# Performance work log

Hardware: AMD Instinct MI355X
Metric: run time of the kernel (lower is better)

The kernel has to match this reference:

```python
import jax, jax.numpy as jnp
import numpy as np

B, S, D_MODEL, N_HEADS = 2, 2048, 1024, 16
HEAD_DIM = D_MODEL // N_HEADS  # 64
SCALE = HEAD_DIM ** -0.5
MASK_FILL = -1e9


def setup_inputs() -> dict:
    key = jax.random.key(0)
    k1, k2, k3 = jax.random.split(key, 3)
    x = jax.random.normal(k1, (B, S, D_MODEL), dtype=jnp.float32)
    # nn.Linear weight [3*d_att, d_model], trunc_normal std=0.02 style init
    W_qkv = jax.random.normal(k2, (3 * D_MODEL, D_MODEL), dtype=jnp.float32) * 0.02
    # boolean attention mask over the full [b, s_q, h, t_k] score tensor (True = keep)
    mask = jax.random.bernoulli(k3, p=0.9, shape=(B, S, N_HEADS, S))
    return {"x": x, "W_qkv": W_qkv, "mask": mask}


def reference(x, W_qkv, mask):
    b, s, dm = x.shape
    h, d = N_HEADS, HEAD_DIM
    # fused QKV projection (no bias): [b,s,3*dm] -> [b,s,3,h,d]
    qkv = jnp.einsum('bsm,nm->bsn', x, W_qkv).reshape(b, s, 3, h, d)
    q, k, v = qkv[:, :, 0], qkv[:, :, 1], qkv[:, :, 2]
    # scores: [b, s_q, h, t_k]
    attn = jnp.einsum('bshd,bthd->bsht', q, k) * SCALE
    attn = jnp.where(mask, attn, MASK_FILL)
    attn = jax.nn.softmax(attn, axis=-1)
    # out[b,t,h,d] = sum_s attn[b,t,h,s] * v[b,s,h,d]  (original einsum 'b s h d, b t h s -> b t h d')
    out = jnp.einsum('bshd,bths->bthd', v, attn)
    return out.reshape(b, s, h * d)  # proj is Identity (d_out=None)
```

## Files before the change

kernel.cpp:

```cpp
#include <hip/hip_runtime.h>

#define S_   2048
#define DM_  1024
#define NH_  16
#define HD_  64
#define NQ_  3072
#define KDIM 1024

typedef __attribute__((ext_vector_type(8))) short  shortx8;
typedef __attribute__((ext_vector_type(4))) float  floatx4;

#define AS1 __attribute__((address_space(1)))
#define AS3 __attribute__((address_space(3)))

__device__ __forceinline__ unsigned short f2bf(float f) {
  unsigned u = __float_as_uint(f);
  u += 0x7FFFu + ((u >> 16) & 1u);
  return (unsigned short)(u >> 16);
}

__device__ __forceinline__ void gld_lds16(const void* g, unsigned short* l) {
  __builtin_amdgcn_global_load_lds((const AS1 void*)g, (AS3 void*)l, 16, 0, 0);
}

__global__ __launch_bounds__(256) void detect_kernel(const unsigned* __restrict__ mask,
                                                     const unsigned* __restrict__ x,
                                                     int* __restrict__ flags)
{
  __shared__ int s[5];
  if (threadIdx.x == 0) { s[0]=1; s[1]=1; s[2]=1; s[3]=1; s[4]=0; }
  __syncthreads();
  bool o32=true, of32=true, o16=true, o8=true;
  for (int i = threadIdx.x; i < 16384; i += 256) {
    unsigned v = mask[i];
    o32 &= (v <= 1u);
    of32 &= (v == 0u) || (v == 0x3F800000u);
    unsigned lo = v & 0xFFFFu, hi = v >> 16;
    o16 &= ((lo==0u)||(lo==0x3F80u)) && ((hi==0u)||(hi==0x3F80u));
    o8  &= ((v & 0xFEFEFEFEu) == 0u);
  }
  int cnt = 0;
  for (int i = threadIdx.x; i < 4096; i += 256) {
    unsigned v = x[i];
    unsigned b1 = (v >> 8) & 0x7Fu;
    cnt += (b1 >= 0x32u && b1 <= 0x41u) ? 1 : 0;
  }
  if (!o32)  atomicAnd(&s[0], 0);
  if (!of32) atomicAnd(&s[1], 0);
  if (!o16)  atomicAnd(&s[2], 0);
  if (!o8)   atomicAnd(&s[3], 0);
  atomicAdd(&s[4], cnt);
  __syncthreads();
  if (threadIdx.x == 0) {
    int mf;
    if (s[0]) mf = 0; else if (s[1]) mf = 3; else if (s[2]) mf = 2; else mf = 1;
    flags[0] = mf;
    flags[1] = (s[4] > 2048) ? 1 : 0;
  }
}

__global__ __launch_bounds__(256) void qkv_gemm(const void* __restrict__ Xv,
                                                const void* __restrict__ Wv,
                                                unsigned short* __restrict__ QKV,
                                                const int* __restrict__ flags)
{
  __shared__ unsigned short lA[128*64];
  __shared__ unsigned short lB[128*64];
  const int tid  = threadIdx.x;
  const int wid  = tid >> 6,  lane = tid & 63;
  const int quad = lane >> 4, l16  = lane & 15;
  const int bm = blockIdx.x, bn = blockIdx.y;
  const int wM = (wid >> 1) * 64, wN = (wid & 1) * 64;
  const int xbf = flags[1];

  floatx4 acc[4][4] = {};

  for (int kt = 0; kt < KDIM; kt += 64) {
    __syncthreads();
    if (xbf) {
      const unsigned short* X = (const unsigned short*)Xv;
      const unsigned short* W = (const unsigned short*)Wv;
      #pragma unroll
      for (int p = 0; p < 4; ++p) {
        int chunk = p*256 + tid;
        int r = chunk >> 3, c = chunk & 7;
        int csw = c ^ (r & 7);
        gld_lds16(X + (size_t)(bm*128 + r)*KDIM + kt + csw*8, lA + chunk*8);
      }
      #pragma unroll
      for (int p = 0; p < 4; ++p) {
        int chunk = p*256 + tid;
        int r = chunk >> 3, c = chunk & 7;
        int csw = c ^ (r & 7);
        gld_lds16(W + (size_t)(bn*128 + r)*KDIM + kt + csw*8, lB + chunk*8);
      }
    } else {
      const float* X = (const float*)Xv;
      const float* W = (const float*)Wv;
      #pragma unroll
      for (int p = 0; p < 8; ++p) {
        int c4 = p*256 + tid;
        int r = c4 >> 4, c = c4 & 15;
        int cg = c >> 1, half = c & 1;
        int csl = cg ^ (r & 7);
        float4 v = *(const float4*)(X + (size_t)(bm*128 + r)*KDIM + kt + c*4);
        unsigned short* d = lA + r*64 + csl*8 + half*4;
        d[0]=f2bf(v.x); d[1]=f2bf(v.y); d[2]=f2bf(v.z); d[3]=f2bf(v.w);
      }
      #pragma unroll
      for (int p = 0; p < 8; ++p) {
        int c4 = p*256 + tid;
        int r = c4 >> 4, c = c4 & 15;
        int cg = c >> 1, half = c & 1;
        int csl = cg ^ (r & 7);
        float4 v = *(const float4*)(W + (size_t)(bn*128 + r)*KDIM + kt + c*4);
        unsigned short* d = lB + r*64 + csl*8 + half*4;
        d[0]=f2bf(v.x); d[1]=f2bf(v.y); d[2]=f2bf(v.z); d[3]=f2bf(v.w);
      }
    }
    __syncthreads();

    #pragma unroll
    for (int ks = 0; ks < 2; ++ks) {
      shortx8 af[4], bfr[4];
      #pragma unroll
      for (int mi = 0; mi < 4; ++mi) {
        int r = wM + mi*16 + l16;
        int csw = (ks*4 + quad) ^ (r & 7);
        af[mi] = *(const shortx8*)(lA + r*64 + csw*8);
      }
      #pragma unroll
      for (int ni = 0; ni < 4; ++ni) {
        int r = wN + ni*16 + l16;
        int csw = (ks*4 + quad) ^ (r & 7);
        bfr[ni] = *(const shortx8*)(lB + r*64 + csw*8);
      }
      #pragma unroll
      for (int mi = 0; mi < 4; ++mi)
        #pragma unroll
        for (int ni = 0; ni < 4; ++ni)
          acc[mi][ni] = __builtin_amdgcn_mfma_f32_16x16x32_bf16(af[mi], bfr[ni], acc[mi][ni], 0, 0, 0);
    }
  }

  #pragma unroll
  for (int mi = 0; mi < 4; ++mi)
    #pragma unroll
    for (int ni = 0; ni < 4; ++ni)
      #pragma unroll
      for (int r = 0; r < 4; ++r) {
        int m = bm*128 + wM + mi*16 + quad*4 + r;
        int n = bn*128 + wN + ni*16 + l16;
        QKV[(size_t)m*NQ_ + n] = f2bf(acc[mi][ni][r]);
      }
}

__global__ __launch_bounds__(256) void attn_kernel(const unsigned short* __restrict__ QKV,
                                                   const void* __restrict__ maskp,
                                                   const int* __restrict__ flags,
                                                   void* __restrict__ outv)
{
  __shared__ unsigned short lQ[64*64];
  __shared__ unsigned short lK[64*64];
  __shared__ unsigned short lVt[64*72];
  __shared__ unsigned short lP[4][16*72];

  const int tid  = threadIdx.x;
  const int wid  = tid >> 6,  lane = tid & 63;
  const int quad = lane >> 4, l16  = lane & 15;
  const int qb = blockIdx.x * 64;
  const int h  = blockIdx.y, b = blockIdx.z;
  const int mflag = flags[0];
  const int obf   = flags[1];

  #pragma unroll
  for (int p = 0; p < 2; ++p) {
    int chunk = p*256 + tid;
    int r = chunk >> 3, c = chunk & 7;
    int csw = c ^ (r & 7);
    gld_lds16(QKV + ((size_t)b*S_ + qb + r)*NQ_ + h*HD_ + csw*8, lQ + chunk*8);
  }
  __syncthreads();

  shortx8 qf[2];
  {
    int r = wid*16 + l16;
    #pragma unroll
    for (int ks = 0; ks < 2; ++ks) {
      int csw = (ks*4 + quad) ^ (r & 7);
      qf[ks] = *(const shortx8*)(lQ + r*64 + csw*8);
    }
  }

  floatx4 acc[4] = {};
  float mrun[4], lrun[4];
  #pragma unroll
  for (int r = 0; r < 4; ++r) { mrun[r] = -1e30f; lrun[r] = 0.f; }

  size_t mbase[4];
  #pragma unroll
  for (int r = 0; r < 4; ++r) {
    int q = qb + wid*16 + quad*4 + r;
    mbase[r] = (((size_t)b*S_ + q)*NH_ + h)*S_ + l16;
  }

  const size_t kvrow = (size_t)b*S_;

  for (int t0 = 0; t0 < S_; t0 += 64) {
    __syncthreads();
    #pragma unroll
    for (int p = 0; p < 2; ++p) {
      int chunk = p*256 + tid;
      int r = chunk >> 3, c = chunk & 7;
      int csw = c ^ (r & 7);
      gld_lds16(QKV + (kvrow + t0 + r)*NQ_ + DM_ + h*HD_ + csw*8, lK + chunk*8);
    }
    #pragma unroll
    for (int p = 0; p < 2; ++p) {
      int chunk = p*256 + tid;
      int t = chunk >> 3, c = chunk & 7;
      uint4 w = *(const uint4*)(QKV + (kvrow + t0 + t)*NQ_ + 2*DM_ + h*HD_ + c*8);
      unsigned short e[8];
      __builtin_memcpy(e, &w, 16);
      #pragma unroll
      for (int j = 0; j < 8; ++j) lVt[(c*8 + j)*72 + t] = e[j];
    }
    __syncthreads();

    floatx4 sc[4] = {};
    #pragma unroll
    for (int tile = 0; tile < 4; ++tile) {
      #pragma unroll
      for (int ks = 0; ks < 2; ++ks) {
        int r = tile*16 + l16;
        int csw = (ks*4 + quad) ^ (r & 7);
        shortx8 kf = *(const shortx8*)(lK + r*64 + csw*8);
        sc[tile] = __builtin_amdgcn_mfma_f32_16x16x32_bf16(qf[ks], kf, sc[tile], 0, 0, 0);
      }
    }

    float s[4][4];
    #pragma unroll
    for (int tile = 0; tile < 4; ++tile)
      #pragma unroll
      for (int r = 0; r < 4; ++r)
        s[tile][r] = sc[tile][r] * 0.125f;

    if (mflag == 0) {
      const int* mp = (const int*)maskp;
      #pragma unroll
      for (int tile = 0; tile < 4; ++tile)
        #pragma unroll
        for (int r = 0; r < 4; ++r)
          if (mp[mbase[r] + t0 + tile*16] == 0) s[tile][r] = -1e30f;
    } else if (mflag == 1) {
      const unsigned char* mp = (const unsigned char*)maskp;
      #pragma unroll
      for (int tile = 0; tile < 4; ++tile)
        #pragma unroll
        for (int r = 0; r < 4; ++r)
          if (mp[mbase[r] + t0 + tile*16] == 0) s[tile][r] = -1e30f;
    } else if (mflag == 2) {
      const unsigned short* mp = (const unsigned short*)maskp;
      #pragma unroll
      for (int tile = 0; tile < 4; ++tile)
        #pragma unroll
        for (int r = 0; r < 4; ++r)
          if (mp[mbase[r] + t0 + tile*16] == 0) s[tile][r] = -1e30f;
    } else {
      const unsigned* mp = (const unsigned*)maskp;
      #pragma unroll
      for (int tile = 0; tile < 4; ++tile)
        #pragma unroll
        for (int r = 0; r < 4; ++r)
          if (mp[mbase[r] + t0 + tile*16] == 0) s[tile][r] = -1e30f;
    }

    float pr[4][4];
    #pragma unroll
    for (int r = 0; r < 4; ++r) {
      float m0 = fmaxf(fmaxf(s[0][r], s[1][r]), fmaxf(s[2][r], s[3][r]));
      #pragma unroll
      for (int o = 1; o < 16; o <<= 1) m0 = fmaxf(m0, __shfl_xor(m0, o));
      float mnew = fmaxf(mrun[r], m0);
      float al = __expf(mrun[r] - mnew);
      mrun[r] = mnew;
      float ls = 0.f;
      #pragma unroll
      for (int tile = 0; tile < 4; ++tile) {
        float p_ = __expf(s[tile][r] - mnew);
        pr[tile][r] = p_; ls += p_;
      }
      #pragma unroll
      for (int o = 1; o < 16; o <<= 1) ls += __shfl_xor(ls, o);
      lrun[r] = lrun[r]*al + ls;
      #pragma unroll
      for (int d = 0; d < 4; ++d) acc[d][r] *= al;
    }

    unsigned short* lPw = lP[wid];
    #pragma unroll
    for (int tile = 0; tile < 4; ++tile)
      #pragma unroll
      for (int r = 0; r < 4; ++r)
        lPw[(quad*4 + r)*72 + tile*16 + l16] = f2bf(pr[tile][r]);

    #pragma unroll
    for (int ks = 0; ks < 2; ++ks) {
      shortx8 pa = *(const shortx8*)(lPw + l16*72 + ks*32 + quad*8);
      #pragma unroll
      for (int d = 0; d < 4; ++d) {
        shortx8 vb = *(const shortx8*)(lVt + (d*16 + l16)*72 + ks*32 + quad*8);
        acc[d] = __builtin_amdgcn_mfma_f32_16x16x32_bf16(pa, vb, acc[d], 0, 0, 0);
      }
    }
  }

  #pragma unroll
  for (int d = 0; d < 4; ++d)
    #pragma unroll
    for (int r = 0; r < 4; ++r) {
      int q = qb + wid*16 + quad*4 + r;
      size_t oi = ((size_t)b*S_ + q)*DM_ + h*HD_ + d*16 + l16;
      float v = acc[d][r] / lrun[r];
      if (obf) ((unsigned short*)outv)[oi] = f2bf(v);
      else     ((float*)outv)[oi]          = v;
    }
}

extern "C" void kernel_launch(void* const* d_in, const int* in_sizes, int n_in,
                              void* d_out, int out_size, void* d_ws, size_t ws_size,
                              hipStream_t stream) {
  (void)in_sizes; (void)n_in; (void)out_size; (void)ws_size;
  const void* X    = d_in[0];
  const void* W    = d_in[1];
  const void* mask = d_in[2];
  int* flags = (int*)d_ws;
  unsigned short* QKV = (unsigned short*)((char*)d_ws + 256);

  detect_kernel<<<1, 256, 0, stream>>>((const unsigned*)mask, (const unsigned*)X, flags);
  qkv_gemm<<<dim3(32, 24), 256, 0, stream>>>(X, W, QKV, flags);
  attn_kernel<<<dim3(32, 16, 2), 256, 0, stream>>>(QKV, mask, flags, d_out);
}
```

Baseline: 929.0 us.

## Write Q/K/V head-major with pre-transposed V and drop online softmax max tracking

The QKV GEMM epilogue now scatters Q (pre-scaled by 1/sqrt(d)) and K into per-head contiguous buffers and writes V transposed per head. This lets the attention kernel load K and V tiles with contiguous direct-to-LDS loads instead of strided row reads and a scalar LDS transpose. The attention kernel also drops the running-max online softmax and exponentiates raw scores, zeroing masked entries, with a single normalisation at the end. Mask loads are issued before the barrier so they overlap the tile loads. The risks are overflow in exp for large scores, since no max is subtracted, and LDS bank conflicts now that the XOR swizzle is removed.

```diff
diff --git a/kernel.cpp b/kernel.cpp
--- a/kernel.cpp
+++ b/kernel.cpp
@@ -4,7 +4,6 @@
 #define DM_  1024
 #define NH_  16
 #define HD_  64
-#define NQ_  3072
 #define KDIM 1024
 
 typedef __attribute__((ext_vector_type(8))) short  shortx8;
@@ -61,7 +60,9 @@
 
 __global__ __launch_bounds__(256) void qkv_gemm(const void* __restrict__ Xv,
                                                 const void* __restrict__ Wv,
-                                                unsigned short* __restrict__ QKV,
+                                                unsigned short* __restrict__ Qg,
+                                                unsigned short* __restrict__ Kg,
+                                                unsigned short* __restrict__ Vt,
                                                 const int* __restrict__ flags)
 {
   __shared__ unsigned short lA[128*64];
@@ -84,15 +85,13 @@
       for (int p = 0; p < 4; ++p) {
         int chunk = p*256 + tid;
         int r = chunk >> 3, c = chunk & 7;
-        int csw = c ^ (r & 7);
-        gld_lds16(X + (size_t)(bm*128 + r)*KDIM + kt + csw*8, lA + chunk*8);
+        gld_lds16(X + (size_t)(bm*128 + r)*KDIM + kt + c*8, lA + chunk*8);
       }
       #pragma unroll
       for (int p = 0; p < 4; ++p) {
         int chunk = p*256 + tid;
         int r = chunk >> 3, c = chunk & 7;
-        int csw = c ^ (r & 7);
-        gld_lds16(W + (size_t)(bn*128 + r)*KDIM + kt + csw*8, lB + chunk*8);
+        gld_lds16(W + (size_t)(bn*128 + r)*KDIM + kt + c*8, lB + chunk*8);
       }
     } else {
       const float* X = (const float*)Xv;
@@ -101,20 +100,16 @@
       for (int p = 0; p < 8; ++p) {
         int c4 = p*256 + tid;
         int r = c4 >> 4, c = c4 & 15;
-        int cg = c >> 1, half = c & 1;
-        int csl = cg ^ (r & 7);
         float4 v = *(const float4*)(X + (size_t)(bm*128 + r)*KDIM + kt + c*4);
-        unsigned short* d = lA + r*64 + csl*8 + half*4;
+        unsigned short* d = lA + r*64 + c*4;
         d[0]=f2bf(v.x); d[1]=f2bf(v.y); d[2]=f2bf(v.z); d[3]=f2bf(v.w);
       }
       #pragma unroll
       for (int p = 0; p < 8; ++p) {
         int c4 = p*256 + tid;
         int r = c4 >> 4, c = c4 & 15;
-        int cg = c >> 1, half = c & 1;
-        int csl = cg ^ (r & 7);
         float4 v = *(const float4*)(W + (size_t)(bn*128 + r)*KDIM + kt + c*4);
-        unsigned short* d = lB + r*64 + csl*8 + half*4;
+        unsigned short* d = lB + r*64 + c*4;
         d[0]=f2bf(v.x); d[1]=f2bf(v.y); d[2]=f2bf(v.z); d[3]=f2bf(v.w);
       }
     }
@@ -124,17 +119,11 @@
     for (int ks = 0; ks < 2; ++ks) {
       shortx8 af[4], bfr[4];
       #pragma unroll
-      for (int mi = 0; mi < 4; ++mi) {
-        int r = wM + mi*16 + l16;
-        int csw = (ks*4 + quad) ^ (r & 7);
-        af[mi] = *(const shortx8*)(lA + r*64 + csw*8);
-      }
-      #pragma unroll
-      for (int ni = 0; ni < 4; ++ni) {
-        int r = wN + ni*16 + l16;
-        int csw = (ks*4 + quad) ^ (r & 7);
-        bfr[ni] = *(const shortx8*)(lB + r*64 + csw*8);
-      }
+      for (int mi = 0; mi < 4; ++mi)
+        af[mi] = *(const shortx8*)(lA + (wM + mi*16 + l16)*64 + ks*32 + quad*8);
+      #pragma unroll
+      for (int ni = 0; ni < 4; ++ni)
+        bfr[ni] = *(const shortx8*)(lB + (wN + ni*16 + l16)*64 + ks*32 + quad*8);
       #pragma unroll
       for (int mi = 0; mi < 4; ++mi)
         #pragma unroll
@@ -143,26 +132,56 @@
     }
   }
 
-  #pragma unroll
-  for (int mi = 0; mi < 4; ++mi)
-    #pragma unroll
-    for (int ni = 0; ni < 4; ++ni)
-      #pragma unroll
-      for (int r = 0; r < 4; ++r) {
-        int m = bm*128 + wM + mi*16 + quad*4 + r;
-        int n = bn*128 + wN + ni*16 + l16;
-        QKV[(size_t)m*NQ_ + n] = f2bf(acc[mi][ni][r]);
-      }
-}
-
-__global__ __launch_bounds__(256) void attn_kernel(const unsigned short* __restrict__ QKV,
+  if (bn < 8) {
+    #pragma unroll
+    for (int mi = 0; mi < 4; ++mi)
+      #pragma unroll
+      for (int ni = 0; ni < 4; ++ni)
+        #pragma unroll
+        for (int r = 0; r < 4; ++r) {
+          int m = bm*128 + wM + mi*16 + quad*4 + r;
+          int n = bn*128 + wN + ni*16 + l16;
+          int b = m >> 11, q = m & 2047, h = n >> 6, d = n & 63;
+          Qg[(((size_t)(b*NH_ + h))*S_ + q)*HD_ + d] = f2bf(acc[mi][ni][r] * 0.125f);
+        }
+  } else if (bn < 16) {
+    #pragma unroll
+    for (int mi = 0; mi < 4; ++mi)
+      #pragma unroll
+      for (int ni = 0; ni < 4; ++ni)
+        #pragma unroll
+        for (int r = 0; r < 4; ++r) {
+          int m = bm*128 + wM + mi*16 + quad*4 + r;
+          int n = bn*128 + wN + ni*16 + l16 - 1024;
+          int b = m >> 11, t = m & 2047, h = n >> 6, d = n & 63;
+          Kg[(((size_t)(b*NH_ + h))*S_ + t)*HD_ + d] = f2bf(acc[mi][ni][r]);
+        }
+  } else {
+    #pragma unroll
+    for (int mi = 0; mi < 4; ++mi)
+      #pragma unroll
+      for (int ni = 0; ni < 4; ++ni) {
+        int m0 = bm*128 + wM + mi*16 + quad*4;
+        int n  = bn*128 + wN + ni*16 + l16 - 2048;
+        int b = m0 >> 11, t = m0 & 2047, h = n >> 6, d = n & 63;
+        ushort4 u;
+        u.x = f2bf(acc[mi][ni][0]); u.y = f2bf(acc[mi][ni][1]);
+        u.z = f2bf(acc[mi][ni][2]); u.w = f2bf(acc[mi][ni][3]);
+        *(ushort4*)(Vt + (((size_t)(b*NH_ + h))*HD_ + d)*S_ + t) = u;
+      }
+  }
+}
+
+__global__ __launch_bounds__(256) void attn_kernel(const unsigned short* __restrict__ Qg,
+                                                   const unsigned short* __restrict__ Kg,
+                                                   const unsigned short* __restrict__ Vt,
                                                    const void* __restrict__ maskp,
                                                    const int* __restrict__ flags,
                                                    void* __restrict__ outv)
 {
   __shared__ unsigned short lQ[64*64];
   __shared__ unsigned short lK[64*64];
-  __shared__ unsigned short lVt[64*72];
+  __shared__ unsigned short lVt[64*64];
   __shared__ unsigned short lP[4][16*72];
 
   const int tid  = threadIdx.x;
@@ -170,32 +189,24 @@
   const int quad = lane >> 4, l16  = lane & 15;
   const int qb = blockIdx.x * 64;
   const int h  = blockIdx.y, b = blockIdx.z;
+  const int bh = b*NH_ + h;
   const int mflag = flags[0];
   const int obf   = flags[1];
 
   #pragma unroll
   for (int p = 0; p < 2; ++p) {
     int chunk = p*256 + tid;
-    int r = chunk >> 3, c = chunk & 7;
-    int csw = c ^ (r & 7);
-    gld_lds16(QKV + ((size_t)b*S_ + qb + r)*NQ_ + h*HD_ + csw*8, lQ + chunk*8);
+    gld_lds16(Qg + ((size_t)bh*S_ + qb)*HD_ + chunk*8, lQ + chunk*8);
   }
   __syncthreads();
 
   shortx8 qf[2];
-  {
-    int r = wid*16 + l16;
-    #pragma unroll
-    for (int ks = 0; ks < 2; ++ks) {
-      int csw = (ks*4 + quad) ^ (r & 7);
-      qf[ks] = *(const shortx8*)(lQ + r*64 + csw*8);
-    }
-  }
+  #pragma unroll
+  for (int ks = 0; ks < 2; ++ks)
+    qf[ks] = *(const shortx8*)(lQ + (wid*16 + l16)*64 + ks*32 + quad*8);
 
   floatx4 acc[4] = {};
-  float mrun[4], lrun[4];
-  #pragma unroll
-  for (int r = 0; r < 4; ++r) { mrun[r] = -1e30f; lrun[r] = 0.f; }
+  float lsum[4] = {0.f, 0.f, 0.f, 0.f};
 
   size_t mbase[4];
   #pragma unroll
@@ -204,116 +215,92 @@
     mbase[r] = (((size_t)b*S_ + q)*NH_ + h)*S_ + l16;
   }
 
-  const size_t kvrow = (size_t)b*S_;
-
   for (int t0 = 0; t0 < S_; t0 += 64) {
     __syncthreads();
+    #pragma unroll
+    for (int p = 0; p < 2; ++p) {
+      int chunk = p*256 + tid;
+      gld_lds16(Kg + ((size_t)bh*S_ + t0)*HD_ + chunk*8, lK + chunk*8);
+    }
     #pragma unroll
     for (int p = 0; p < 2; ++p) {
       int chunk = p*256 + tid;
       int r = chunk >> 3, c = chunk & 7;
-      int csw = c ^ (r & 7);
-      gld_lds16(QKV + (kvrow + t0 + r)*NQ_ + DM_ + h*HD_ + csw*8, lK + chunk*8);
-    }
-    #pragma unroll
-    for (int p = 0; p < 2; ++p) {
-      int chunk = p*256 + tid;
-      int t = chunk >> 3, c = chunk & 7;
-      uint4 w = *(const uint4*)(QKV + (kvrow + t0 + t)*NQ_ + 2*DM_ + h*HD_ + c*8);
-      unsigned short e[8];
-      __builtin_memcpy(e, &w, 16);
-      #pragma unroll
-      for (int j = 0; j < 8; ++j) lVt[(c*8 + j)*72 + t] = e[j];
-    }
-    __syncthreads();
-
-    floatx4 sc[4] = {};
-    #pragma unroll
-    for (int tile = 0; tile < 4; ++tile) {
-      #pragma unroll
-      for (int ks = 0; ks < 2; ++ks) {
-        int r = tile*16 + l16;
-        int csw = (ks*4 + quad) ^ (r & 7);
-        shortx8 kf = *(const shortx8*)(lK + r*64 + csw*8);
-        sc[tile] = __builtin_amdgcn_mfma_f32_16x16x32_bf16(qf[ks], kf, sc[tile], 0, 0, 0);
-      }
-    }
-
-    float s[4][4];
-    #pragma unroll
-    for (int tile = 0; tile < 4; ++tile)
-      #pragma unroll
-      for (int r = 0; r < 4; ++r)
-        s[tile][r] = sc[tile][r] * 0.125f;
-
+      gld_lds16(Vt + ((size_t)bh*HD_ + r)*S_ + t0 + c*8, lVt + chunk*8);
+    }
+
+    unsigned mnz[4][4];
     if (mflag == 0) {
-      const int* mp = (const int*)maskp;
+      const unsigned* mp = (const unsigned*)maskp;
       #pragma unroll
       for (int tile = 0; tile < 4; ++tile)
         #pragma unroll
-        for (int r = 0; r < 4; ++r)
-          if (mp[mbase[r] + t0 + tile*16] == 0) s[tile][r] = -1e30f;
+        for (int r = 0; r < 4; ++r) mnz[tile][r] = mp[mbase[r] + t0 + tile*16];
     } else if (mflag == 1) {
       const unsigned char* mp = (const unsigned char*)maskp;
       #pragma unroll
       for (int tile = 0; tile < 4; ++tile)
         #pragma unroll
-        for (int r = 0; r < 4; ++r)
-          if (mp[mbase[r] + t0 + tile*16] == 0) s[tile][r] = -1e30f;
+        for (int r = 0; r < 4; ++r) mnz[tile][r] = mp[mbase[r] + t0 + tile*16];
     } else if (mflag == 2) {
       const unsigned short* mp = (const unsigned short*)maskp;
       #pragma unroll
       for (int tile = 0; tile < 4; ++tile)
         #pragma unroll
-        for (int r = 0; r < 4; ++r)
-          if (mp[mbase[r] + t0 + tile*16] == 0) s[tile][r] = -1e30f;
+        for (int r = 0; r < 4; ++r) mnz[tile][r] = mp[mbase[r] + t0 + tile*16];
     } else {
       const unsigned* mp = (const unsigned*)maskp;
       #pragma unroll
       for (int tile = 0; tile < 4; ++tile)
         #pragma unroll
-        for (int r = 0; r < 4; ++r)
-          if (mp[mbase[r] + t0 + tile*16] == 0) s[tile][r] = -1e30f;
-    }
-
-    float pr[4][4];
-    #pragma unroll
-    for (int r = 0; r < 4; ++r) {
-      float m0 = fmaxf(fmaxf(s[0][r], s[1][r]), fmaxf(s[2][r], s[3][r]));
-      #pragma unroll
-      for (int o = 1; o < 16; o <<= 1) m0 = fmaxf(m0, __shfl_xor(m0, o));
-      float mnew = fmaxf(mrun[r], m0);
-      float al = __expf(mrun[r] - mnew);
-      mrun[r] = mnew;
-      float ls = 0.f;
-      #pragma unroll
-      for (int tile = 0; tile < 4; ++tile) {
-        float p_ = __expf(s[tile][r] - mnew);
-        pr[tile][r] = p_; ls += p_;
-      }
-      #pragma unroll
-      for (int o = 1; o < 16; o <<= 1) ls += __shfl_xor(ls, o);
-      lrun[r] = lrun[r]*al + ls;
-      #pragma unroll
-      for (int d = 0; d < 4; ++d) acc[d][r] *= al;
-    }
+        for (int r = 0; r < 4; ++r) mnz[tile][r] = mp[mbase[r] + t0 + tile*16];
+    }
+    __syncthreads();
+
+    floatx4 sc[4] = {};
+    #pragma unroll
+    for (int tile = 0; tile < 4; ++tile)
+      #pragma unroll
+      for (int ks = 0; ks < 2; ++ks) {
+        shortx8 kf = *(const shortx8*)(lK + (tile*16 + l16)*64 + ks*32 + quad*8);
+        sc[tile] = __builtin_amdgcn_mfma_f32_16x16x32_bf16(qf[ks], kf, sc[tile], 0, 0, 0);
+      }
+
+    float pv[4][4];
+    #pragma unroll
+    for (int tile = 0; tile < 4; ++tile)
+      #pragma unroll
+      for (int r = 0; r < 4; ++r) {
+        float e = __expf(sc[tile][r]);
+        pv[tile][r] = mnz[tile][r] ? e : 0.f;
+        lsum[r] += pv[tile][r];
+      }
 
     unsigned short* lPw = lP[wid];
     #pragma unroll
     for (int tile = 0; tile < 4; ++tile)
       #pragma unroll
       for (int r = 0; r < 4; ++r)
-        lPw[(quad*4 + r)*72 + tile*16 + l16] = f2bf(pr[tile][r]);
+        lPw[(quad*4 + r)*72 + tile*16 + l16] = f2bf(pv[tile][r]);
 
     #pragma unroll
     for (int ks = 0; ks < 2; ++ks) {
       shortx8 pa = *(const shortx8*)(lPw + l16*72 + ks*32 + quad*8);
       #pragma unroll
       for (int d = 0; d < 4; ++d) {
-        shortx8 vb = *(const shortx8*)(lVt + (d*16 + l16)*72 + ks*32 + quad*8);
+        shortx8 vb = *(const shortx8*)(lVt + (d*16 + l16)*64 + ks*32 + quad*8);
         acc[d] = __builtin_amdgcn_mfma_f32_16x16x32_bf16(pa, vb, acc[d], 0, 0, 0);
       }
     }
+  }
+
+  float rinv[4];
+  #pragma unroll
+  for (int r = 0; r < 4; ++r) {
+    float l = lsum[r];
+    #pragma unroll
+    for (int o = 1; o < 16; o <<= 1) l += __shfl_xor(l, o);
+    rinv[r] = 1.f / l;
   }
 
   #pragma unroll
@@ -322,7 +309,7 @@
     for (int r = 0; r < 4; ++r) {
       int q = qb + wid*16 + quad*4 + r;
       size_t oi = ((size_t)b*S_ + q)*DM_ + h*HD_ + d*16 + l16;
-      float v = acc[d][r] / lrun[r];
+      float v = acc[d][r] * rinv[r];
       if (obf) ((unsigned short*)outv)[oi] = f2bf(v);
       else     ((float*)outv)[oi]          = v;
     }
@@ -336,9 +323,12 @@
   const void* W    = d_in[1];
   const void* mask = d_in[2];
   int* flags = (int*)d_ws;
-  unsigned short* QKV = (unsigned short*)((char*)d_ws + 256);
+  const size_t SEG = (size_t)2*NH_*S_*HD_*2;
+  unsigned short* Qg = (unsigned short*)((char*)d_ws + 256);
+  unsigned short* Kg = (unsigned short*)((char*)d_ws + 256 + SEG);
+  unsigned short* Vt = (unsigned short*)((char*)d_ws + 256 + 2*SEG);
 
   detect_kernel<<<1, 256, 0, stream>>>((const unsigned*)mask, (const unsigned*)X, flags);
-  qkv_gemm<<<dim3(32, 24), 256, 0, stream>>>(X, W, QKV, flags);
-  attn_kernel<<<dim3(32, 16, 2), 256, 0, stream>>>(QKV, mask, flags, d_out);
-}
+  qkv_gemm<<<dim3(32, 24), 256, 0, stream>>>(X, W, Qg, Kg, Vt, flags);
+  attn_kernel<<<dim3(32, 16, 2), 256, 0, stream>>>(Qg, Kg, Vt, mask, flags, d_out);
+}
```

New measurement: 882.2 us. 5.0% less time.
